# Kernel tuning notes

Hardware: AMD Instinct MI355X
Metric: run time of the kernel (lower is better)

The kernel has to match this reference:

```python
import jax, jax.numpy as jnp
import numpy as np

WEIGHT = 0.01
EPS = 1e-12  # torch F.normalize default eps


def setup_inputs() -> dict:
    key = jax.random.key(0)
    factor = jax.random.normal(key, (65536, 2048), dtype=jnp.float32)
    return {"factor": factor}


def reference(factor):
    # L2-normalize rows (torch F.normalize, dim=1): x / max(||x||, eps)
    norms = jnp.linalg.norm(factor, axis=1, keepdims=True)
    f = factor / jnp.maximum(norms, EPS)
    N = f.shape[0]
    # diag(f @ f.T, +1)[i] = <f_i, f_{i+1}>; diag(.., -1) is identical by symmetry.
    adj = jnp.sum(f[:-1] * f[1:], axis=1)  # [N-1]
    positive1 = jnp.sum(adj) / (N - 1)
    positive2 = positive1  # gram matrix is symmetric
    time_diff = positive1 + positive2
    return -WEIGHT * time_diff
```

## Files before the change

kernel.cpp:

```cpp
#include <hip/hip_runtime.h>
#include <math.h>


#define N_ROWS 65536
#define N_COLS 2048
#define ROWS_PER_WAVE 16

__global__ __launch_bounds__(256) void tcr_pass1(const float* __restrict__ x,
                                                 float* __restrict__ sq,
                                                 float* __restrict__ cross) {
    const int wid  = (blockIdx.x * 256 + threadIdx.x) >> 6;
    const int lane = threadIdx.x & 63;
    const long r0 = (long)wid * ROWS_PER_WAVE;

    const float4* rowp = (const float4*)x;

    float4 prev[8];
    {
        long base = r0 * 512 + lane;
        #pragma unroll
        for (int k = 0; k < 8; ++k) prev[k] = rowp[base + (long)k * 64];
    }
    {
        float s = 0.f;
        #pragma unroll
        for (int k = 0; k < 8; ++k)
            s += prev[k].x * prev[k].x + prev[k].y * prev[k].y +
                 prev[k].z * prev[k].z + prev[k].w * prev[k].w;
        #pragma unroll
        for (int off = 32; off; off >>= 1) s += __shfl_xor(s, off, 64);
        if (lane == 0) sq[r0] = s;
    }

    const int rend = (int)r0 + ROWS_PER_WAVE;
    for (int r = (int)r0 + 1; r <= rend; ++r) {
        if (r >= N_ROWS) break;
        float4 cur[8];
        long base = (long)r * 512 + lane;
        #pragma unroll
        for (int k = 0; k < 8; ++k) cur[k] = rowp[base + (long)k * 64];

        float sqp = 0.f, crp = 0.f;
        #pragma unroll
        for (int k = 0; k < 8; ++k) {
            sqp += cur[k].x * cur[k].x + cur[k].y * cur[k].y +
                   cur[k].z * cur[k].z + cur[k].w * cur[k].w;
            crp += prev[k].x * cur[k].x + prev[k].y * cur[k].y +
                   prev[k].z * cur[k].z + prev[k].w * cur[k].w;
            prev[k] = cur[k];
        }
        #pragma unroll
        for (int off = 32; off; off >>= 1) {
            sqp += __shfl_xor(sqp, off, 64);
            crp += __shfl_xor(crp, off, 64);
        }
        if (lane == 0) {
            cross[r - 1] = crp;
            if (r < rend) sq[r] = sqp;
        }
    }
}

__global__ __launch_bounds__(256) void tcr_pass2(const float* __restrict__ sq,
                                                 const float* __restrict__ cross,
                                                 float* __restrict__ out) {
    const int tid    = blockIdx.x * 256 + threadIdx.x;
    const int stride = gridDim.x * 256;
    double acc = 0.0;
    for (int i = tid; i < N_ROWS - 1; i += stride) {
        double ni = fmax(sqrt((double)sq[i]),     1e-12);
        double nj = fmax(sqrt((double)sq[i + 1]), 1e-12);
        acc += (double)cross[i] / (ni * nj);
    }
    __shared__ double sd[256];
    sd[threadIdx.x] = acc;
    __syncthreads();
    for (int s = 128; s; s >>= 1) {
        if (threadIdx.x < s) sd[threadIdx.x] += sd[threadIdx.x + s];
        __syncthreads();
    }
    if (threadIdx.x == 0) {
        double partial = sd[0] * (-2.0 * 0.01 / (double)(N_ROWS - 1));
        atomicAdd(out, (float)partial);
    }
}

extern "C" void kernel_launch(void* const* d_in, const int* in_sizes, int n_in,
                              void* d_out, int out_size, void* d_ws, size_t ws_size,
                              hipStream_t stream) {
    const float* factor = (const float*)d_in[0];
    float* out = (float*)d_out;

    float* sq    = (float*)d_ws;
    float* cross = sq + N_ROWS;

    const int n_waves  = N_ROWS / ROWS_PER_WAVE;
    const int n_blocks = n_waves / 4;
    tcr_pass1<<<n_blocks, 256, 0, stream>>>(factor, sq, cross);

    hipMemsetAsync(d_out, 0, sizeof(float), stream);

    tcr_pass2<<<64, 256, 0, stream>>>(sq, cross, out);
}
```

Baseline: 685.3 us.

## Prefetch next row in pass1 and collapse pass2 into single block without memset

Pass1 now software-pipelines row loads, issuing the load for row i+1 before computing the square sum and dot product of the current pair, and fully unrolls the per-wave loop with FMA chains. Pass2 becomes one 1024-thread block that does float math, a wave-shuffle reduction and a direct store, which removes the memset and the atomic. The prefetch raises register pressure (three 8-float4 buffers), and the kernel is still bound by streaming the 512 MB input.

After: 694.0 us. About the same (+1.3%).

```diff
diff --git a/kernel.cpp b/kernel.cpp
--- a/kernel.cpp
+++ b/kernel.cpp
@@ -4,84 +4,96 @@
 
 #define N_ROWS 65536
 #define N_COLS 2048
-#define ROWS_PER_WAVE 16
+#define RPW 16
+
+__device__ __forceinline__ void load_row(float4 dst[8], const float4* __restrict__ rowp,
+                                         int r, int lane) {
+    const float4* p = rowp + ((long)r << 9) + lane;
+    #pragma unroll
+    for (int k = 0; k < 8; ++k) dst[k] = p[(long)k * 64];
+}
+
+__device__ __forceinline__ float row_sq(const float4 a[8]) {
+    float s = 0.f;
+    #pragma unroll
+    for (int k = 0; k < 8; ++k)
+        s = fmaf(a[k].x, a[k].x, fmaf(a[k].y, a[k].y,
+            fmaf(a[k].z, a[k].z, fmaf(a[k].w, a[k].w, s))));
+    return s;
+}
+
+__device__ __forceinline__ float row_dot(const float4 a[8], const float4 b[8]) {
+    float s = 0.f;
+    #pragma unroll
+    for (int k = 0; k < 8; ++k)
+        s = fmaf(a[k].x, b[k].x, fmaf(a[k].y, b[k].y,
+            fmaf(a[k].z, b[k].z, fmaf(a[k].w, b[k].w, s))));
+    return s;
+}
 
 __global__ __launch_bounds__(256) void tcr_pass1(const float* __restrict__ x,
                                                  float* __restrict__ sq,
                                                  float* __restrict__ cross) {
     const int wid  = (blockIdx.x * 256 + threadIdx.x) >> 6;
     const int lane = threadIdx.x & 63;
-    const long r0 = (long)wid * ROWS_PER_WAVE;
-
+    const int r0   = wid * RPW;
     const float4* rowp = (const float4*)x;
 
-    float4 prev[8];
-    {
-        long base = r0 * 512 + lane;
-        #pragma unroll
-        for (int k = 0; k < 8; ++k) prev[k] = rowp[base + (long)k * 64];
-    }
-    {
-        float s = 0.f;
-        #pragma unroll
-        for (int k = 0; k < 8; ++k)
-            s += prev[k].x * prev[k].x + prev[k].y * prev[k].y +
-                 prev[k].z * prev[k].z + prev[k].w * prev[k].w;
-        #pragma unroll
-        for (int off = 32; off; off >>= 1) s += __shfl_xor(s, off, 64);
-        if (lane == 0) sq[r0] = s;
-    }
+    float4 A[8], B[8];
+    load_row(A, rowp, r0, lane);
+    load_row(B, rowp, r0 + 1, lane);
 
-    const int rend = (int)r0 + ROWS_PER_WAVE;
-    for (int r = (int)r0 + 1; r <= rend; ++r) {
-        if (r >= N_ROWS) break;
-        float4 cur[8];
-        long base = (long)r * 512 + lane;
-        #pragma unroll
-        for (int k = 0; k < 8; ++k) cur[k] = rowp[base + (long)k * 64];
+    float s0 = row_sq(A);
+    #pragma unroll
+    for (int off = 32; off; off >>= 1) s0 += __shfl_xor(s0, off, 64);
+    if (lane == 0) sq[r0] = s0;
 
-        float sqp = 0.f, crp = 0.f;
-        #pragma unroll
-        for (int k = 0; k < 8; ++k) {
-            sqp += cur[k].x * cur[k].x + cur[k].y * cur[k].y +
-                   cur[k].z * cur[k].z + cur[k].w * cur[k].w;
-            crp += prev[k].x * cur[k].x + prev[k].y * cur[k].y +
-                   prev[k].z * cur[k].z + prev[k].w * cur[k].w;
-            prev[k] = cur[k];
+    #pragma unroll
+    for (int i = 1; i <= RPW; ++i) {
+        float4 C[8];
+        if (i < RPW) {
+            int rn = r0 + i + 1;
+            if (rn > N_ROWS - 1) rn = N_ROWS - 1;
+            load_row(C, rowp, rn, lane);
         }
+        float sb = row_sq(B);
+        float cr = row_dot(A, B);
         #pragma unroll
         for (int off = 32; off; off >>= 1) {
-            sqp += __shfl_xor(sqp, off, 64);
-            crp += __shfl_xor(crp, off, 64);
+            sb += __shfl_xor(sb, off, 64);
+            cr += __shfl_xor(cr, off, 64);
         }
         if (lane == 0) {
-            cross[r - 1] = crp;
-            if (r < rend) sq[r] = sqp;
+            cross[r0 + i - 1] = cr;
+            if (i < RPW) sq[r0 + i] = sb;
+        }
+        if (i < RPW) {
+            #pragma unroll
+            for (int k = 0; k < 8; ++k) { A[k] = B[k]; B[k] = C[k]; }
         }
     }
 }
 
-__global__ __launch_bounds__(256) void tcr_pass2(const float* __restrict__ sq,
-                                                 const float* __restrict__ cross,
-                                                 float* __restrict__ out) {
-    const int tid    = blockIdx.x * 256 + threadIdx.x;
-    const int stride = gridDim.x * 256;
+__global__ __launch_bounds__(1024) void tcr_pass2(const float* __restrict__ sq,
+                                                  const float* __restrict__ cross,
+                                                  float* __restrict__ out) {
+    const int tid = threadIdx.x;
     double acc = 0.0;
-    for (int i = tid; i < N_ROWS - 1; i += stride) {
-        double ni = fmax(sqrt((double)sq[i]),     1e-12);
-        double nj = fmax(sqrt((double)sq[i + 1]), 1e-12);
-        acc += (double)cross[i] / (ni * nj);
+    for (int i = tid; i < N_ROWS - 1; i += 1024) {
+        float ni = fmaxf(sqrtf(sq[i]),     1e-12f);
+        float nj = fmaxf(sqrtf(sq[i + 1]), 1e-12f);
+        acc += (double)(cross[i] / (ni * nj));
     }
-    __shared__ double sd[256];
-    sd[threadIdx.x] = acc;
+    #pragma unroll
+    for (int off = 32; off; off >>= 1) acc += __shfl_xor(acc, off, 64);
+    __shared__ double sd[16];
+    if ((tid & 63) == 0) sd[tid >> 6] = acc;
     __syncthreads();
-    for (int s = 128; s; s >>= 1) {
-        if (threadIdx.x < s) sd[threadIdx.x] += sd[threadIdx.x + s];
-        __syncthreads();
-    }
-    if (threadIdx.x == 0) {
-        double partial = sd[0] * (-2.0 * 0.01 / (double)(N_ROWS - 1));
-        atomicAdd(out, (float)partial);
+    if (tid == 0) {
+        double t = 0.0;
+        #pragma unroll
+        for (int w = 0; w < 16; ++w) t += sd[w];
+        out[0] = (float)(t * (-2.0 * 0.01 / (double)(N_ROWS - 1)));
     }
 }
 
@@ -94,11 +106,8 @@
     float* sq    = (float*)d_ws;
     float* cross = sq + N_ROWS;
 
-    const int n_waves  = N_ROWS / ROWS_PER_WAVE;
+    const int n_waves  = N_ROWS / RPW;
     const int n_blocks = n_waves / 4;
     tcr_pass1<<<n_blocks, 256, 0, stream>>>(factor, sq, cross);
-
-    hipMemsetAsync(d_out, 0, sizeof(float), stream);
-
-    tcr_pass2<<<64, 256, 0, stream>>>(sq, cross, out);
+    tcr_pass2<<<1, 1024, 0, stream>>>(sq, cross, out);
 }
```
